# Kernel optimization log

Measured on AMD Instinct MI355X. Metric: run time of the kernel, lower is better.

Reference implementation:

```python
import jax, jax.numpy as jnp
import numpy as np

NMUL = 16
NASH = 3
NEARZERO = 1e-5
TIMESTEP_D = 1.0
LENF = 15

PARAM_BOUNDS = [
    ("schaake_const", 0.0, 0.1), ("smcmax", 0.3, 0.6), ("soil_depth", 0.5, 3.0),
    ("wltsmc", 0.05, 0.2), ("satpsi", 0.01, 0.5), ("bb", 2.0, 12.0),
    ("mult", 100.0, 2000.0), ("satdk", 1e-7, 1e-4), ("slop", 0.0, 1.0),
    ("max_gw_storage", 0.01, 0.5), ("Cgw", 1e-6, 1e-3), ("expon", 1.0, 8.0),
    ("K_nash", 0.01, 0.5),
]
ROUT_BOUNDS = [("rout_a", 0.0, 2.9), ("rout_b", 0.0, 6.5)]


def setup_inputs() -> dict:
    key = jax.random.key(0)
    k1, k2 = jax.random.split(key)
    T, B = 730, 2048
    # prcp ~ U[0,20) mm/d, pet ~ U[0,8) mm/d
    x_phy = jax.random.uniform(k1, (T, B, 2), dtype=jnp.float32) * jnp.array([20.0, 8.0], jnp.float32)
    n_static = len(PARAM_BOUNDS) * NMUL + len(ROUT_BOUNDS)  # 210
    phy_static = jax.random.uniform(k2, (B, n_static), dtype=jnp.float32)
    return {"x_phy": x_phy, "phy_static": phy_static}


def _cfe_forward(x_phy, phy_static):
    T, B, _ = x_phy.shape
    n_phys = len(PARAM_BOUNDS)
    # descale: change_param_range(p, [lb, ub]) = p * (ub - lb) + lb
    phys = phy_static[:, : n_phys * NMUL].reshape(B, n_phys, NMUL)
    prm = {name: phys[:, i, :] * (ub - lb) + lb for i, (name, lb, ub) in enumerate(PARAM_BOUNDS)}
    route_raw = phy_static[:, n_phys * NMUL :]
    rout = {name: route_raw[:, i] * (ub - lb) + lb for i, (name, lb, ub) in enumerate(ROUT_BOUNDS)}

    P = jnp.repeat(x_phy[:, :, 0:1], NMUL, axis=2)    # [T,B,NMUL]
    PET = jnp.repeat(x_phy[:, :, 1:2], NMUL, axis=2)  # [T,B,NMUL]

    soil0 = jnp.full((B, NMUL), 0.05, jnp.float32)
    gw0 = jnp.full((B, NMUL), 0.01, jnp.float32)
    nash0 = jnp.full((B, NMUL, NASH), NEARZERO, jnp.float32)

    max_soil = prm["smcmax"] * prm["soil_depth"]
    # Clapp-Hornberger field-capacity threshold from satpsi, bb
    fc_frac = jnp.clip((prm["satpsi"] / prm["soil_depth"]) ** (1.0 / prm["bb"]), 0.0, 1.0)
    fc_threshold = prm["smcmax"] * fc_frac * prm["soil_depth"]

    def step(carry, forc):
        soil, gw, nash = carry
        p, pet = forc
        # --- ET: first from rainfall, then Budyko-type from soil ---
        et_rain = jnp.minimum(p, pet)
        p_rem = p - et_rain
        pet_rem = pet - et_rain
        smc = soil / prm["soil_depth"]
        budyko = jnp.clip((smc - prm["wltsmc"]) / (prm["smcmax"] - prm["wltsmc"] + NEARZERO), 0.0, 1.0)
        aet_soil = jnp.minimum(pet_rem * budyko, jnp.maximum(soil - NEARZERO, 0.0))
        soil = soil - aet_soil
        aet = et_rain + aet_soil
        # --- Schaake infiltration / runoff partitioning ---
        deficit = jnp.maximum(max_soil - soil, 0.0)
        infil_cap = deficit * (1.0 - jnp.exp(-prm["schaake_const"] * TIMESTEP_D))
        runoff = p_rem * p_rem / (p_rem + infil_cap + NEARZERO)
        runoff = jnp.minimum(runoff, p_rem)
        infiltration = jnp.minimum(p_rem - runoff, deficit)
        runoff = p_rem - infiltration
        soil = soil + infiltration
        # --- soil dual-outlet nonlinear reservoir (percolation + lateral) ---
        above = jnp.maximum(soil - fc_threshold, 0.0)
        frac = above / jnp.maximum(max_soil - fc_threshold, NEARZERO)
        perc = prm["satdk"] * prm["mult"] * TIMESTEP_D * frac
        lat = prm["satdk"] * prm["mult"] * prm["slop"] * TIMESTEP_D * frac
        tot = perc + lat
        scale = jnp.minimum(1.0, above / jnp.maximum(tot, NEARZERO))
        perc = perc * scale
        lat = lat * scale
        soil = soil - perc - lat
        # --- groundwater exponential reservoir ---
        gw = gw + perc
        q_gw = prm["Cgw"] * jnp.expm1(prm["expon"] * jnp.clip(gw / prm["max_gw_storage"], 0.0, 1.0))
        q_gw = jnp.clip(q_gw, 0.0, jnp.maximum(gw - NEARZERO, 0.0))
        gw = gw - q_gw
        # --- Nash cascade routing of lateral flow (3 linear reservoirs) ---
        inflow = lat
        K = prm["K_nash"]
        new_nash = []
        for i in range(NASH):
            s = nash[..., i] + inflow
            out = K * s
            new_nash.append(s - out)
            inflow = out
        nash = jnp.stack(new_nash, axis=-1)
        q_lat = inflow
        q_sim = runoff + q_lat + q_gw
        return (soil, gw, nash), (q_sim, runoff, q_lat, q_gw, aet, soil, gw)

    _, outs = jax.lax.scan(step, (soil0, gw0, nash0), (P, PET))
    q_sim = outs[0]                 # [T,B,NMUL]
    q_avg = q_sim.mean(-1)          # [T,B]  multi-model averaging

    # --- gamma unit-hydrograph routing (uh_gamma + causal uh_conv) ---
    a = jax.nn.relu(rout["rout_a"])[:, None] + 0.1    # [B,1]
    th = jax.nn.relu(rout["rout_b"])[:, None] + 0.5   # [B,1]
    t = (jnp.arange(LENF, dtype=jnp.float32) + 0.5)[None, :]  # [1,LENF]
    w = t ** (a - 1.0) * jnp.exp(-t / th) / (jnp.exp(jax.lax.lgamma(a)) * th ** a)
    w = w / w.sum(1, keepdims=True)                    # [B,LENF]
    xp = jnp.pad(q_avg, ((LENF - 1, 0), (0, 0)))       # causal pad on time axis
    stream = sum(
        w[None, :, j] * jax.lax.dynamic_slice_in_dim(xp, LENF - 1 - j, T, 0)
        for j in range(LENF)
    )
    return stream[..., None]  # [T,B,1] routed streamflow


def reference(x_phy, phy_static):
    return _cfe_forward(x_phy, phy_static)
```

## Files before the change

kernel.cpp:

```cpp
#include <hip/hip_runtime.h>
#include <math.h>


constexpr int T_STEPS = 730;
constexpr int BATCH   = 2048;
constexpr int NMULC   = 16;
constexpr int LENFC   = 15;
constexpr int NPHYS   = 13;
constexpr int NSTAT   = NPHYS * NMULC + 2;
constexpr float NZ    = 1e-5f;
constexpr float INV_NZ= 1e5f;
constexpr int NCH     = 2;
constexpr int LPB     = 8;
constexpr int TB      = 15;
constexpr int T_MAIN  = 720;

typedef float v2f __attribute__((ext_vector_type(2)));

__device__ __forceinline__ float frcp(float x) { return __builtin_amdgcn_rcpf(x); }
__device__ __forceinline__ v2f v2(float s) { return (v2f){s, s}; }
__device__ __forceinline__ v2f vmin(v2f a, v2f b) { return __builtin_elementwise_min(a, b); }
__device__ __forceinline__ v2f vmax(v2f a, v2f b) { return __builtin_elementwise_max(a, b); }

__device__ __forceinline__ float dpp_sum8(float x) {
    int v;
    v = __builtin_amdgcn_update_dpp(0, __float_as_int(x), 0xB1, 0xF, 0xF, true);
    x += __int_as_float(v);
    v = __builtin_amdgcn_update_dpp(0, __float_as_int(x), 0x4E, 0xF, 0xF, true);
    x += __int_as_float(v);
    v = __builtin_amdgcn_update_dpp(0, __float_as_int(x), 0x141, 0xF, 0xF, true);
    x += __int_as_float(v);
    return x;
}

struct Prm {
    v2f k1, k2, ms, fc, ic, cc, pc, lc, sc, e2, Km, Kk, Cg, ig;
    float w[LENFC];
};
struct St { v2f soil, gw, n0, n1, n2; };

template <int SLOT>
__device__ __forceinline__ float substep(const Prm& P, St& S,
                                         float (&ring)[LENFC], const float2 fv)
{
    const float p = fv.x, pet = fv.y;
    const float et      = fminf(p, pet);
    const float p_rem   = p - et;
    const float pet_rem = pet - et;
    const float prem_nz = p_rem + NZ;
    const float prem_sq = p_rem * p_rem;

    v2f budyko = S.soil * P.k1 + P.k2;
    budyko = vmin(vmax(budyko, v2(0.0f)), v2(1.0f));
    const v2f aet = vmin(v2(pet_rem) * budyko, S.soil - v2(NZ));
    v2f so = S.soil - aet;

    const v2f deficit = P.ms - so;
    const v2f den     = deficit * P.ic + v2(prem_nz);
    v2f rden; rden.x = frcp(den.x); rden.y = frcp(den.y);
    const v2f runoff0 = v2(prem_sq) * rden;
    const v2f infil   = vmin(v2(p_rem) - runoff0, deficit);
    const v2f runoff  = v2(p_rem) - infil;
    so += infil;

    const v2f above = vmax(so - P.fc, v2(0.0f));
    const v2f asc   = vmin(above * P.sc, above * above * v2(INV_NZ));
    const v2f lat   = P.lc * asc;
    so = so - P.cc * asc;
    S.soil = so;

    v2f g = P.pc * asc + S.gw;
    const v2f ratio = vmin(g * P.ig, v2(1.0f));
    v2f ex;
    ex.x = __builtin_amdgcn_exp2f(P.e2.x * ratio.x);
    ex.y = __builtin_amdgcn_exp2f(P.e2.y * ratio.y);
    const v2f qg0 = P.Cg * ex - P.Cg;
    const v2f qg  = vmin(qg0, g - v2(NZ));
    S.gw = g - qg;

    const v2f s0 = S.n0 + lat;
    const v2f s1 = P.Kk * s0 + S.n1;
    const v2f s2 = P.Kk * s1 + S.n2;
    const v2f o2 = P.Kk * s2;
    S.n0 = P.Km * s0; S.n1 = P.Km * s1; S.n2 = P.Km * s2;

    const v2f qv = runoff + o2 + qg;
    const float qsum = qv.x + qv.y;

    ring[SLOT] = qsum;
    float c0 = 0.0f, c1 = 0.0f, c2 = 0.0f, c3 = 0.0f;
    #pragma unroll
    for (int j = 0; j < LENFC; j += 4) {
        c0 = fmaf(P.w[j], ring[(SLOT - j + 15) % 15], c0);
        if (j + 1 < LENFC) c1 = fmaf(P.w[j + 1], ring[(SLOT - j - 1 + 30) % 15], c1);
        if (j + 2 < LENFC) c2 = fmaf(P.w[j + 2], ring[(SLOT - j - 2 + 30) % 15], c2);
        if (j + 3 < LENFC) c3 = fmaf(P.w[j + 3], ring[(SLOT - j - 3 + 30) % 15], c3);
    }
    return (c0 + c1) + (c2 + c3);
}

#define SUBST(s, FBUF, TBASE) {                                              \
    const float acc = substep<(s)>(P, S, ring, FBUF[(s)]);                   \
    const float r = dpp_sum8(acc);                                           \
    if (lane0) out[((TBASE) + (s)) * BATCH + b] = r; }
#define DO15(FBUF, TBASE) \
    SUBST(0,FBUF,TBASE) SUBST(1,FBUF,TBASE) SUBST(2,FBUF,TBASE)  \
    SUBST(3,FBUF,TBASE) SUBST(4,FBUF,TBASE) SUBST(5,FBUF,TBASE)  \
    SUBST(6,FBUF,TBASE) SUBST(7,FBUF,TBASE) SUBST(8,FBUF,TBASE)  \
    SUBST(9,FBUF,TBASE) SUBST(10,FBUF,TBASE) SUBST(11,FBUF,TBASE)\
    SUBST(12,FBUF,TBASE) SUBST(13,FBUF,TBASE) SUBST(14,FBUF,TBASE)
#define DO10(FBUF, TBASE) \
    SUBST(0,FBUF,TBASE) SUBST(1,FBUF,TBASE) SUBST(2,FBUF,TBASE)  \
    SUBST(3,FBUF,TBASE) SUBST(4,FBUF,TBASE) SUBST(5,FBUF,TBASE)  \
    SUBST(6,FBUF,TBASE) SUBST(7,FBUF,TBASE) SUBST(8,FBUF,TBASE)  \
    SUBST(9,FBUF,TBASE)

__global__ __launch_bounds__(64, 1)
void cfe_kernel(const float* __restrict__ x,
                const float* __restrict__ ps,
                float* __restrict__ out)
{
    const int tid = blockIdx.x * 64 + threadIdx.x;
    const int b   = tid >> 3;
    const int m0  = tid & 7;
    const bool lane0 = (m0 == 0);

    const float* __restrict__ row = ps + b * NSTAT;

    Prm P;
    #pragma unroll
    for (int c = 0; c < NCH; ++c) {
        const int m = m0 + c * 8;
        const float schaake    = row[ 0*NMULC + m] * 0.1f;
        const float smcmax     = row[ 1*NMULC + m] * 0.3f   + 0.3f;
        const float soil_depth = row[ 2*NMULC + m] * 2.5f   + 0.5f;
        const float wltsmc     = row[ 3*NMULC + m] * 0.15f  + 0.05f;
        const float satpsi     = row[ 4*NMULC + m] * 0.49f  + 0.01f;
        const float bb_        = row[ 5*NMULC + m] * 10.0f  + 2.0f;
        const float multp      = row[ 6*NMULC + m] * 1900.0f+ 100.0f;
        const float satdk      = row[ 7*NMULC + m] * (1e-4f - 1e-7f) + 1e-7f;
        const float slop       = row[ 8*NMULC + m];
        const float max_gw     = row[ 9*NMULC + m] * 0.49f  + 0.01f;
        const float Cgw        = row[10*NMULC + m] * (1e-3f - 1e-6f) + 1e-6f;
        const float expon      = row[11*NMULC + m] * 7.0f   + 1.0f;
        const float K          = row[12*NMULC + m] * 0.49f  + 0.01f;

        const float inv_sd  = 1.0f / soil_depth;
        const float bud_den = 1.0f / (smcmax - wltsmc + NZ);
        const float ms      = smcmax * soil_depth;
        float fc_frac = powf(satpsi * inv_sd, 1.0f / bb_);
        fc_frac = fminf(fmaxf(fc_frac, 0.0f), 1.0f);
        const float fc      = smcmax * fc_frac * soil_depth;
        const float sm      = satdk * multp;
        const float sml     = sm * slop;
        const float inv_mft = 1.0f / fmaxf(ms - fc, NZ);
        const float ccv     = inv_mft * (sm + sml);

        P.k1[c] = inv_sd * bud_den;
        P.k2[c] = -wltsmc * bud_den;
        P.ms[c] = ms;
        P.fc[c] = fc;
        P.ic[c] = 1.0f - expf(-schaake);
        P.cc[c] = ccv;
        P.pc[c] = sm  * inv_mft;
        P.lc[c] = sml * inv_mft;
        P.sc[c] = fminf(1.0f, 1.0f / ccv);
        P.e2[c] = expon * 1.442695041f;
        P.Km[c] = 1.0f - K;
        P.Kk[c] = K;
        P.Cg[c] = Cgw;
        P.ig[c] = 1.0f / max_gw;
    }

    {
        const float rout_a = row[NPHYS*NMULC + 0] * 2.9f;
        const float rout_b = row[NPHYS*NMULC + 1] * 6.5f;
        const float a  = fmaxf(rout_a, 0.0f) + 0.1f;
        const float th = fmaxf(rout_b, 0.0f) + 0.5f;
        float wsum = 0.0f;
        #pragma unroll
        for (int j = 0; j < LENFC; ++j) {
            const float tj = (float)j + 0.5f;
            P.w[j] = powf(tj, a - 1.0f) * expf(-tj / th);
            wsum += P.w[j];
        }
        const float wscale = 1.0f / (wsum * (float)NMULC);
        #pragma unroll
        for (int j = 0; j < LENFC; ++j) P.w[j] *= wscale;
    }

    St S;
    S.soil = v2(0.05f); S.gw = v2(0.01f);
    S.n0 = v2(NZ); S.n1 = v2(NZ); S.n2 = v2(NZ);
    float ring[LENFC];
    #pragma unroll
    for (int j = 0; j < LENFC; ++j) ring[j] = 0.0f;

    const float2* __restrict__ xp = (const float2*)x;

    float2 fA[TB], fB[TB];
    #pragma unroll
    for (int s = 0; s < TB; ++s) fA[s] = xp[s * BATCH + b];

    #pragma unroll 1
    for (int tb = 0; tb < T_MAIN; tb += 2 * TB) {
        #pragma unroll
        for (int s = 0; s < TB; ++s) {
            int t = tb + TB + s; if (t > T_STEPS - 1) t = T_STEPS - 1;
            fB[s] = xp[t * BATCH + b];
        }
        DO15(fA, tb)
        #pragma unroll
        for (int s = 0; s < TB; ++s) {
            int t = tb + 2 * TB + s; if (t > T_STEPS - 1) t = T_STEPS - 1;
            fA[s] = xp[t * BATCH + b];
        }
        DO15(fB, tb + TB)
    }

    DO10(fA, T_MAIN)
}

extern "C" void kernel_launch(void* const* d_in, const int* in_sizes, int n_in,
                              void* d_out, int out_size, void* d_ws, size_t ws_size,
                              hipStream_t stream) {
    const float* x_phy      = (const float*)d_in[0];
    const float* phy_static = (const float*)d_in[1];
    float* out = (float*)d_out;

    const int total = BATCH * LPB;
    const int block = 64;
    const int grid  = total / block;
    cfe_kernel<<<grid, block, 0, stream>>>(x_phy, phy_static, out);
}
```

Measured before the change: 156.0 us.

## Split NMUL members across two waves with LDS cross-wave reduction per timestep

Each thread now simulates one multiplier member instead of two packed in a float2 vector, and a block becomes two wavefronts (128 threads) covering 8 basins. Per-step partial sums are reduced within each wave by DPP, then combined across the two waves through a double-buffered shared-memory array with a __syncthreads. The store is deferred by one step so the reduction of step t-1 can overlap step t's compute. The aim is to halve the serial per-thread dependency chain over 730 steps by doubling thread count, at the cost of a block barrier every timestep and duplicated routing-convolution work.

```diff
diff --git a/kernel.cpp b/kernel.cpp
--- a/kernel.cpp
+++ b/kernel.cpp
@@ -10,17 +10,11 @@
 constexpr int NSTAT   = NPHYS * NMULC + 2;
 constexpr float NZ    = 1e-5f;
 constexpr float INV_NZ= 1e5f;
-constexpr int NCH     = 2;
-constexpr int LPB     = 8;
+constexpr int BPB     = 8;
 constexpr int TB      = 15;
 constexpr int T_MAIN  = 720;
 
-typedef float v2f __attribute__((ext_vector_type(2)));
-
 __device__ __forceinline__ float frcp(float x) { return __builtin_amdgcn_rcpf(x); }
-__device__ __forceinline__ v2f v2(float s) { return (v2f){s, s}; }
-__device__ __forceinline__ v2f vmin(v2f a, v2f b) { return __builtin_elementwise_min(a, b); }
-__device__ __forceinline__ v2f vmax(v2f a, v2f b) { return __builtin_elementwise_max(a, b); }
 
 __device__ __forceinline__ float dpp_sum8(float x) {
     int v;
@@ -34,10 +28,10 @@
 }
 
 struct Prm {
-    v2f k1, k2, ms, fc, ic, cc, pc, lc, sc, e2, Km, Kk, Cg, ig;
+    float k1, k2, ms, fc, ic, cc, pc, lc, sc, e2, Km, Kk, Cg, ig;
     float w[LENFC];
 };
-struct St { v2f soil, gw, n0, n1, n2; };
+struct St { float soil, gw, n0, n1, n2; };
 
 template <int SLOT>
 __device__ __forceinline__ float substep(const Prm& P, St& S,
@@ -50,42 +44,35 @@
     const float prem_nz = p_rem + NZ;
     const float prem_sq = p_rem * p_rem;
 
-    v2f budyko = S.soil * P.k1 + P.k2;
-    budyko = vmin(vmax(budyko, v2(0.0f)), v2(1.0f));
-    const v2f aet = vmin(v2(pet_rem) * budyko, S.soil - v2(NZ));
-    v2f so = S.soil - aet;
-
-    const v2f deficit = P.ms - so;
-    const v2f den     = deficit * P.ic + v2(prem_nz);
-    v2f rden; rden.x = frcp(den.x); rden.y = frcp(den.y);
-    const v2f runoff0 = v2(prem_sq) * rden;
-    const v2f infil   = vmin(v2(p_rem) - runoff0, deficit);
-    const v2f runoff  = v2(p_rem) - infil;
+    float budyko = fmaf(S.soil, P.k1, P.k2);
+    budyko = fminf(fmaxf(budyko, 0.0f), 1.0f);
+    const float aet = fminf(pet_rem * budyko, S.soil - NZ);
+    float so = S.soil - aet;
+
+    const float deficit = P.ms - so;
+    const float den     = fmaf(deficit, P.ic, prem_nz);
+    const float runoff0 = prem_sq * frcp(den);
+    const float infil   = fminf(p_rem - runoff0, deficit);
+    const float runoff  = p_rem - infil;
     so += infil;
 
-    const v2f above = vmax(so - P.fc, v2(0.0f));
-    const v2f asc   = vmin(above * P.sc, above * above * v2(INV_NZ));
-    const v2f lat   = P.lc * asc;
-    so = so - P.cc * asc;
+    const float above = fmaxf(so - P.fc, 0.0f);
+    const float asc   = fminf(above * P.sc, above * above * INV_NZ);
+    const float lat   = P.lc * asc;
+    so = fmaf(-P.cc, asc, so);
     S.soil = so;
 
-    v2f g = P.pc * asc + S.gw;
-    const v2f ratio = vmin(g * P.ig, v2(1.0f));
-    v2f ex;
-    ex.x = __builtin_amdgcn_exp2f(P.e2.x * ratio.x);
-    ex.y = __builtin_amdgcn_exp2f(P.e2.y * ratio.y);
-    const v2f qg0 = P.Cg * ex - P.Cg;
-    const v2f qg  = vmin(qg0, g - v2(NZ));
+    float g = fmaf(P.pc, asc, S.gw);
+    const float ratio = fminf(g * P.ig, 1.0f);
+    const float qg0   = fmaf(P.Cg, __builtin_amdgcn_exp2f(P.e2 * ratio), -P.Cg);
+    const float qg    = fminf(qg0, g - NZ);
     S.gw = g - qg;
 
-    const v2f s0 = S.n0 + lat;
-    const v2f s1 = P.Kk * s0 + S.n1;
-    const v2f s2 = P.Kk * s1 + S.n2;
-    const v2f o2 = P.Kk * s2;
+    const float s0 = S.n0 + lat;            const float s1 = fmaf(P.Kk, s0, S.n1);
+    const float s2 = fmaf(P.Kk, s1, S.n2);  const float o2 = P.Kk * s2;
     S.n0 = P.Km * s0; S.n1 = P.Km * s1; S.n2 = P.Km * s2;
 
-    const v2f qv = runoff + o2 + qg;
-    const float qsum = qv.x + qv.y;
+    const float qsum = runoff + o2 + qg;
 
     ring[SLOT] = qsum;
     float c0 = 0.0f, c1 = 0.0f, c2 = 0.0f, c3 = 0.0f;
@@ -99,10 +86,14 @@
     return (c0 + c1) + (c2 + c3);
 }
 
-#define SUBST(s, FBUF, TBASE) {                                              \
-    const float acc = substep<(s)>(P, S, ring, FBUF[(s)]);                   \
-    const float r = dpp_sum8(acc);                                           \
-    if (lane0) out[((TBASE) + (s)) * BATCH + b] = r; }
+#define SUBST(s, FBUF, TBASE) {                                                 \
+    const float r = dpp_sum8(s_prev);                                           \
+    if (red0) smx[(s) & 1][wv * BPB + bb] = r;                                  \
+    __syncthreads();                                                            \
+    if (st0 && ((TBASE) + (s)) > 0)                                             \
+        out[((TBASE) + (s) - 1) * BATCH + b] =                                  \
+            smx[(s) & 1][bb] + smx[(s) & 1][BPB + bb];                          \
+    s_prev = substep<(s)>(P, S, ring, FBUF[(s)]); }
 #define DO15(FBUF, TBASE) \
     SUBST(0,FBUF,TBASE) SUBST(1,FBUF,TBASE) SUBST(2,FBUF,TBASE)  \
     SUBST(3,FBUF,TBASE) SUBST(4,FBUF,TBASE) SUBST(5,FBUF,TBASE)  \
@@ -115,22 +106,26 @@
     SUBST(6,FBUF,TBASE) SUBST(7,FBUF,TBASE) SUBST(8,FBUF,TBASE)  \
     SUBST(9,FBUF,TBASE)
 
-__global__ __launch_bounds__(64, 1)
+__global__ __launch_bounds__(128, 1)
 void cfe_kernel(const float* __restrict__ x,
                 const float* __restrict__ ps,
                 float* __restrict__ out)
 {
-    const int tid = blockIdx.x * 64 + threadIdx.x;
-    const int b   = tid >> 3;
-    const int m0  = tid & 7;
-    const bool lane0 = (m0 == 0);
+    __shared__ float smx[2][2 * BPB];
+
+    const int lt   = threadIdx.x;
+    const int lane = lt & 63;
+    const int wv   = lt >> 6;
+    const int bb   = lane >> 3;
+    const int b    = blockIdx.x * BPB + bb;
+    const int m    = (lane & 7) + wv * 8;
+    const bool red0 = ((lane & 7) == 0);
+    const bool st0  = red0 && (wv == 0);
 
     const float* __restrict__ row = ps + b * NSTAT;
 
     Prm P;
-    #pragma unroll
-    for (int c = 0; c < NCH; ++c) {
-        const int m = m0 + c * 8;
+    {
         const float schaake    = row[ 0*NMULC + m] * 0.1f;
         const float smcmax     = row[ 1*NMULC + m] * 0.3f   + 0.3f;
         const float soil_depth = row[ 2*NMULC + m] * 2.5f   + 0.5f;
@@ -156,20 +151,20 @@
         const float inv_mft = 1.0f / fmaxf(ms - fc, NZ);
         const float ccv     = inv_mft * (sm + sml);
 
-        P.k1[c] = inv_sd * bud_den;
-        P.k2[c] = -wltsmc * bud_den;
-        P.ms[c] = ms;
-        P.fc[c] = fc;
-        P.ic[c] = 1.0f - expf(-schaake);
-        P.cc[c] = ccv;
-        P.pc[c] = sm  * inv_mft;
-        P.lc[c] = sml * inv_mft;
-        P.sc[c] = fminf(1.0f, 1.0f / ccv);
-        P.e2[c] = expon * 1.442695041f;
-        P.Km[c] = 1.0f - K;
-        P.Kk[c] = K;
-        P.Cg[c] = Cgw;
-        P.ig[c] = 1.0f / max_gw;
+        P.k1 = inv_sd * bud_den;
+        P.k2 = -wltsmc * bud_den;
+        P.ms = ms;
+        P.fc = fc;
+        P.ic = 1.0f - expf(-schaake);
+        P.cc = ccv;
+        P.pc = sm  * inv_mft;
+        P.lc = sml * inv_mft;
+        P.sc = fminf(1.0f, 1.0f / ccv);
+        P.e2 = expon * 1.442695041f;
+        P.Km = 1.0f - K;
+        P.Kk = K;
+        P.Cg = Cgw;
+        P.ig = 1.0f / max_gw;
     }
 
     {
@@ -190,8 +185,7 @@
     }
 
     St S;
-    S.soil = v2(0.05f); S.gw = v2(0.01f);
-    S.n0 = v2(NZ); S.n1 = v2(NZ); S.n2 = v2(NZ);
+    S.soil = 0.05f; S.gw = 0.01f; S.n0 = NZ; S.n1 = NZ; S.n2 = NZ;
     float ring[LENFC];
     #pragma unroll
     for (int j = 0; j < LENFC; ++j) ring[j] = 0.0f;
@@ -201,6 +195,8 @@
     float2 fA[TB], fB[TB];
     #pragma unroll
     for (int s = 0; s < TB; ++s) fA[s] = xp[s * BATCH + b];
+
+    float s_prev = 0.0f;
 
     #pragma unroll 1
     for (int tb = 0; tb < T_MAIN; tb += 2 * TB) {
@@ -219,6 +215,13 @@
     }
 
     DO10(fA, T_MAIN)
+
+    {
+        const float r = dpp_sum8(s_prev);
+        if (red0) smx[0][wv * BPB + bb] = r;
+        __syncthreads();
+        if (st0) out[(T_STEPS - 1) * BATCH + b] = smx[0][bb] + smx[0][BPB + bb];
+    }
 }
 
 extern "C" void kernel_launch(void* const* d_in, const int* in_sizes, int n_in,
@@ -228,8 +231,6 @@
     const float* phy_static = (const float*)d_in[1];
     float* out = (float*)d_out;
 
-    const int total = BATCH * LPB;
-    const int block = 64;
-    const int grid  = total / block;
-    cfe_kernel<<<grid, block, 0, stream>>>(x_phy, phy_static, out);
-}
+    const int grid = BATCH / BPB;
+    cfe_kernel<<<grid, 128, 0, stream>>>(x_phy, phy_static, out);
+}
```

Result: slower. 186.2 us (+19.4%).
